# Kernel tuning notes

Measured on AMD Instinct MI355X. Metric: run time of the kernel, lower is better.

The kernel has to match this reference:

```python
import jax, jax.numpy as jnp
import numpy as np

N = 20000          # nodes
E_RAND = 320000    # random edges (avg degree 16)
E = E_RAND + N     # + self loops (no 0-in-degree nodes)
F_IN = 128
H1, D1 = 8, 32     # layer-1 heads / per-head dim
N_CLS = 40
NEG_SLOPE = 0.2


def setup_inputs() -> dict:
    key = jax.random.key(0)
    ks = jax.random.split(key, 9)
    x = jax.random.normal(ks[0], (N, F_IN), jnp.float32)
    src = jnp.concatenate([jax.random.randint(ks[1], (E_RAND,), 0, N),
                           jnp.arange(N)]).astype(jnp.int32)
    dst = jnp.concatenate([jax.random.randint(ks[2], (E_RAND,), 0, N),
                           jnp.arange(N)]).astype(jnp.int32)
    W1 = jax.random.normal(ks[3], (F_IN, H1 * D1), jnp.float32) / np.sqrt(F_IN)
    attn_l1 = jax.random.normal(ks[4], (H1, D1), jnp.float32) * 0.1
    attn_r1 = jax.random.normal(ks[5], (H1, D1), jnp.float32) * 0.1
    W2 = jax.random.normal(ks[6], (H1 * D1, N_CLS), jnp.float32) / np.sqrt(H1 * D1)
    attn_l2 = jax.random.normal(ks[7], (1, N_CLS), jnp.float32) * 0.1
    attn_r2 = jax.random.normal(ks[8], (1, N_CLS), jnp.float32) * 0.1
    return {"x": x, "W1": W1, "attn_l1": attn_l1, "attn_r1": attn_r1,
            "W2": W2, "attn_l2": attn_l2, "attn_r2": attn_r2,
            "src": src, "dst": dst}


def gat_layer(h, W, attn_l, attn_r, src, dst, n_nodes):
    """DGL GATConv (aggr='mean' path), eval mode (dropout = identity)."""
    H, D = attn_l.shape
    ft = (h @ W).reshape(-1, H, D)                 # [N, H, D]
    el = jnp.sum(ft * attn_l, axis=-1)             # [N, H]
    er = jnp.sum(ft * attn_r, axis=-1)             # [N, H]
    e = jax.nn.leaky_relu(el[src] + er[dst], NEG_SLOPE)   # [E, H]
    # ragged softmax over incoming edges of each dst node
    m = jax.ops.segment_max(e, dst, num_segments=n_nodes)
    m = jnp.where(jnp.isfinite(m), m, 0.0)         # guard empty segments
    ex = jnp.exp(e - m[dst])                       # [E, H]
    s = jax.ops.segment_sum(ex, dst, num_segments=n_nodes)
    alpha = ex / jnp.maximum(s[dst], 1e-16)        # [E, H]
    # weighted sum of src features
    out = jax.ops.segment_sum(ft[src] * alpha[:, :, None], dst,
                              num_segments=n_nodes)  # [N, H, D]
    return out


def reference(x, W1, attn_l1, attn_r1, W2, attn_l2, attn_r2, src, dst):
    h = gat_layer(x, W1, attn_l1, attn_r1, src, dst, N)   # [N, 8, 32]
    h = jax.nn.relu(h).reshape(N, H1 * D1)                # flatten(1)
    out = gat_layer(h, W2, attn_l2, attn_r2, src, dst, N) # [N, 1, 40]
    return out.mean(axis=1)                               # [N, 40]
```

## Files before the change

### kernel.cpp

```cpp
#include <hip/hip_runtime.h>
#include <hip/hip_fp16.h>

#define FIN 128
#define F1 256
#define H1N 8
#define D1N 32
#define NCLS 40
#define FT2P 64
#define W2PITCH 260
#define NEG 0.2f

static __device__ __forceinline__ float leaky(float x){ return x >= 0.f ? x : NEG*x; }

__global__ void k_hist(const int* __restrict__ dst, int* __restrict__ deg, int E){
    int e = blockIdx.x*256 + threadIdx.x;
    if (e < E) atomicAdd(&deg[dst[e]], 1);
}

__global__ void k_scan1(const int* __restrict__ deg, int* __restrict__ rowptr,
                        int* __restrict__ bsum, int n){
    __shared__ int s[256];
    int t = threadIdx.x;
    int i = blockIdx.x*256 + t;
    int v = (i < n) ? deg[i] : 0;
    s[t] = v;
    __syncthreads();
    for (int off=1; off<256; off<<=1){
        int y = (t >= off) ? s[t-off] : 0;
        __syncthreads();
        if (t >= off) s[t] += y;
        __syncthreads();
    }
    if (i < n) rowptr[i] = s[t] - v;
    if (t == 255) bsum[blockIdx.x] = s[255];
}

__global__ void k_scan2(int* __restrict__ rowptr, const int* __restrict__ bsum,
                        int n, int E){
    int b = blockIdx.x;
    int l = threadIdx.x & 63;
    int v = 0;
    for (int j = l; j < b; j += 64) v += bsum[j];
    for (int msk=1; msk<64; msk<<=1) v += __shfl_xor(v, msk);
    int i = b*256 + threadIdx.x;
    if (i < n) rowptr[i] += v;
    else if (i == n) rowptr[n] = E;
}

__global__ void k_scatter(const int* __restrict__ src, const int* __restrict__ dst,
                          const int* __restrict__ rowptr, int* __restrict__ deg,
                          int* __restrict__ adj, int E){
    int e = blockIdx.x*256 + threadIdx.x;
    if (e < E){
        int d = dst[e];
        int pos = atomicSub(&deg[d], 1) - 1;
        adj[rowptr[d] + pos] = src[e];
    }
}

__global__ __launch_bounds__(256) void k_gemm1(const float* __restrict__ X,
                                               const float* __restrict__ W,
                                               const float* __restrict__ al,
                                               const float* __restrict__ ar,
                                               __half* __restrict__ FT,
                                               float* __restrict__ el,
                                               float* __restrict__ er, int M){
    __shared__ float As[32][68];
    __shared__ float Bs[32][68];
    int t = threadIdx.x;
    int bx = blockIdx.x & 3;
    int by = blockIdx.x >> 2;
    int m0 = by*64, n0 = bx*64;
    int ty = t >> 4, tx = t & 15;
    float acc[4][4] = {};
    for (int k0 = 0; k0 < FIN; k0 += 32){
        #pragma unroll
        for (int p=0;p<2;p++){
            int f = t + p*256;
            int m = f >> 3;
            int kq = f & 7;
            int row = m0 + m;
            float4 v = make_float4(0.f,0.f,0.f,0.f);
            if (row < M) v = *(const float4*)&X[row*FIN + k0 + kq*4];
            As[kq*4+0][m] = v.x; As[kq*4+1][m] = v.y;
            As[kq*4+2][m] = v.z; As[kq*4+3][m] = v.w;
        }
        #pragma unroll
        for (int p=0;p<2;p++){
            int f = t + p*256;
            int kk = f >> 4;
            int nq = f & 15;
            float4 v = *(const float4*)&W[(size_t)(k0+kk)*F1 + n0 + nq*4];
            *(float4*)&Bs[kk][nq*4] = v;
        }
        __syncthreads();
        #pragma unroll
        for (int kk=0; kk<32; kk++){
            float4 a4 = *(const float4*)&As[kk][ty*4];
            float4 b4 = *(const float4*)&Bs[kk][tx*4];
            float av[4] = {a4.x,a4.y,a4.z,a4.w};
            float bv[4] = {b4.x,b4.y,b4.z,b4.w};
            #pragma unroll
            for (int r=0;r<4;r++)
                #pragma unroll
                for (int c=0;c<4;c++)
                    acc[r][c] = fmaf(av[r], bv[c], acc[r][c]);
        }
        __syncthreads();
    }
    int h = (bx<<1) + (tx>>3);
    int basew = h*D1N + (tx&7)*4;
    float4 wl = *(const float4*)&al[basew];
    float4 wr = *(const float4*)&ar[basew];
    float pl[4], pr[4];
    #pragma unroll
    for (int r=0;r<4;r++){
        pl[r] = acc[r][0]*wl.x + acc[r][1]*wl.y + acc[r][2]*wl.z + acc[r][3]*wl.w;
        pr[r] = acc[r][0]*wr.x + acc[r][1]*wr.y + acc[r][2]*wr.z + acc[r][3]*wr.w;
    }
    #pragma unroll
    for (int msk=1; msk<8; msk<<=1){
        #pragma unroll
        for (int r=0;r<4;r++){
            pl[r] += __shfl_xor(pl[r], msk);
            pr[r] += __shfl_xor(pr[r], msk);
        }
    }
    #pragma unroll
    for (int r=0;r<4;r++){
        int row = m0 + ty*4 + r;
        if (row < M){
            union { uint2 u; __half2 h2[2]; } P;
            P.h2[0] = __floats2half2_rn(acc[r][0], acc[r][1]);
            P.h2[1] = __floats2half2_rn(acc[r][2], acc[r][3]);
            *(uint2*)&FT[(size_t)row*F1 + n0 + tx*4] = P.u;
            if ((tx & 7) == 0){
                el[row*H1N + h] = pl[r];
                er[row*H1N + h] = pr[r];
            }
        }
    }
}

__global__ __launch_bounds__(256) void k_agg1(const __half* __restrict__ FT,
                      const float* __restrict__ el, const float* __restrict__ er,
                      const float* __restrict__ W2,
                      const float* __restrict__ al2, const float* __restrict__ ar2,
                      const int* __restrict__ rowptr, const int* __restrict__ adj,
                      __half* __restrict__ FT2, float* __restrict__ el2,
                      float* __restrict__ er2, int n, int nwTot){
    __shared__ __half W2h[40*W2PITCH];
    __shared__ float  hst[4][260];
    int t = threadIdx.x;
    for (int e = t; e < 256*40; e += 256){
        int k = e / 40, c = e - k*40;
        W2h[c*W2PITCH + k] = __float2half_rn(W2[e]);
    }
    __syncthreads();

    int w = t >> 6, l = t & 63;
    int h = l & 7, je = l >> 3;
    int h2 = l >> 3;
    int c = (l < 40) ? l : (l - 40);
    float keep = (l < NCLS) ? 1.f : 0.f;
    float a2l = al2[c], a2r = ar2[c];
    const __half* wrow = &W2h[c*W2PITCH];
    float* hp = &hst[w][0];

    for (int node = blockIdx.x*4 + w; node < n; node += nwTot){
        int rs = rowptr[node];
        int deg = rowptr[node+1] - rs;

        float erh = er[node*H1N + h];
        float m = -1e30f, ssum = 0.f;
        for (int j0 = 0; j0 < deg; j0 += 8){
            int j = j0 + je;
            if (j < deg){
                int s = adj[rs + j];
                float e = leaky(el[s*H1N + h] + erh);
                if (e > m){ ssum = ssum*__expf(m - e) + 1.f; m = e; }
                else ssum += __expf(e - m);
            }
        }
        #pragma unroll
        for (int msk=8; msk<64; msk<<=1){
            float m2 = __shfl_xor(m, msk);
            float s2 = __shfl_xor(ssum, msk);
            float nm = fmaxf(m, m2);
            ssum = ssum*__expf(m - nm) + s2*__expf(m2 - nm);
            m = nm;
        }

        float m2 = __shfl(m, h2);
        float s2 = __shfl(ssum, h2);
        float inv = 1.f / fmaxf(s2, 1e-16f);
        float erh2 = er[node*H1N + h2];
        float ax=0.f, ay=0.f, az=0.f, aw=0.f;
        int j = 0;
        for (; j + 8 <= deg; j += 8){
            int sv[8];
            #pragma unroll
            for (int i=0;i<8;i++) sv[i] = adj[rs+j+i];
            float av[8];
            #pragma unroll
            for (int i=0;i<8;i++)
                av[i] = __expf(leaky(el[sv[i]*H1N + h2] + erh2) - m2);
            #pragma unroll
            for (int i=0;i<8;i++){
                union { uint2 u; __half2 h2v[2]; } U;
                U.u = *(const uint2*)&FT[(size_t)sv[i]*F1 + l*4];
                float2 f01 = __half22float2(U.h2v[0]);
                float2 f23 = __half22float2(U.h2v[1]);
                ax = fmaf(av[i], f01.x, ax); ay = fmaf(av[i], f01.y, ay);
                az = fmaf(av[i], f23.x, az); aw = fmaf(av[i], f23.y, aw);
            }
        }
        for (; j < deg; j++){
            int s = adj[rs + j];
            float a = __expf(leaky(el[s*H1N + h2] + erh2) - m2);
            union { uint2 u; __half2 h2v[2]; } U;
            U.u = *(const uint2*)&FT[(size_t)s*F1 + l*4];
            float2 f01 = __half22float2(U.h2v[0]);
            float2 f23 = __half22float2(U.h2v[1]);
            ax = fmaf(a, f01.x, ax); ay = fmaf(a, f01.y, ay);
            az = fmaf(a, f23.x, az); aw = fmaf(a, f23.y, aw);
        }
        ax = fmaxf(ax*inv, 0.f); ay = fmaxf(ay*inv, 0.f);
        az = fmaxf(az*inv, 0.f); aw = fmaxf(aw*inv, 0.f);

        *(float4*)&hp[l*4] = make_float4(ax, ay, az, aw);
        __builtin_amdgcn_wave_barrier();
        asm volatile("s_waitcnt lgkmcnt(0)" ::: "memory");
        float out = 0.f;
        #pragma unroll 8
        for (int k0 = 0; k0 < 64; k0++){
            float4 hv = *(const float4*)&hp[k0*4];
            __half2 wa = *(const __half2*)&wrow[k0*4];
            __half2 wb = *(const __half2*)&wrow[k0*4+2];
            float2 fa = __half22float2(wa), fb = __half22float2(wb);
            out = fmaf(hv.x, fa.x, out); out = fmaf(hv.y, fa.y, out);
            out = fmaf(hv.z, fb.x, out); out = fmaf(hv.w, fb.y, out);
        }
        __builtin_amdgcn_wave_barrier();
        float pl = keep * out * a2l;
        float pr = keep * out * a2r;
        #pragma unroll
        for (int msk=1; msk<64; msk<<=1){
            pl += __shfl_xor(pl, msk);
            pr += __shfl_xor(pr, msk);
        }
        if (l == 0){ el2[node] = pl; er2[node] = pr; }
        if (l < NCLS) FT2[(size_t)node*FT2P + l] = __float2half_rn(out);
    }
}

__global__ __launch_bounds__(256) void k_agg2(const __half* __restrict__ FT2,
                      const float* __restrict__ el, const float* __restrict__ er,
                      const int* __restrict__ rowptr, const int* __restrict__ adj,
                      float* __restrict__ out, int n){
    int node = (blockIdx.x*256 + threadIdx.x) >> 6;
    int l = threadIdx.x & 63;
    if (node >= n) return;
    int rs = rowptr[node];
    int deg = rowptr[node+1] - rs;
    float ern = er[node];
    float m = -1e30f, ssum = 0.f;
    for (int j = l; j < deg; j += 64){
        int s = adj[rs + j];
        float e = leaky(el[s] + ern);
        if (e > m){ ssum = ssum*__expf(m - e) + 1.f; m = e; }
        else ssum += __expf(e - m);
    }
    #pragma unroll
    for (int msk=1; msk<64; msk<<=1){
        float mm = __shfl_xor(m, msk);
        float s2 = __shfl_xor(ssum, msk);
        float nm = fmaxf(m, mm);
        ssum = ssum*__expf(m - nm) + s2*__expf(mm - nm);
        m = nm;
    }
    float inv = 1.f / fmaxf(ssum, 1e-16f);
    float acc = 0.f;
    int j = 0;
    for (; j + 8 <= deg; j += 8){
        int sv[8];
        #pragma unroll
        for (int i=0;i<8;i++) sv[i] = adj[rs+j+i];
        float av[8];
        #pragma unroll
        for (int i=0;i<8;i++)
            av[i] = __expf(leaky(el[sv[i]] + ern) - m);
        if (l < NCLS){
            #pragma unroll
            for (int i=0;i<8;i++){
                float f = __half2float(FT2[(size_t)sv[i]*FT2P + l]);
                acc = fmaf(av[i], f, acc);
            }
        }
    }
    for (; j < deg; j++){
        int s = adj[rs + j];
        float a = __expf(leaky(el[s] + ern) - m);
        if (l < NCLS) acc = fmaf(a, __half2float(FT2[(size_t)s*FT2P + l]), acc);
    }
    if (l < NCLS) out[(size_t)node*NCLS + l] = acc * inv;
}

extern "C" void kernel_launch(void* const* d_in, const int* in_sizes, int n_in,
                              void* d_out, int out_size, void* d_ws, size_t ws_size,
                              hipStream_t stream){
    const float* x   = (const float*)d_in[0];
    const float* W1  = (const float*)d_in[1];
    const float* al1 = (const float*)d_in[2];
    const float* ar1 = (const float*)d_in[3];
    const float* W2  = (const float*)d_in[4];
    const float* al2 = (const float*)d_in[5];
    const float* ar2 = (const float*)d_in[6];
    const int*   src = (const int*)d_in[7];
    const int*   dst = (const int*)d_in[8];
    int E = in_sizes[7];
    int n = in_sizes[0] / FIN;

    char* ws = (char*)d_ws;
    size_t off = 0;
    auto alloc = [&](size_t bytes)->void*{
        void* p = ws + off; off += (bytes + 255) & ~(size_t)255; return p;
    };
    __half* ft1h  = (__half*)alloc((size_t)n*F1*2);
    __half* ft2h  = (__half*)alloc((size_t)n*FT2P*2);
    float*  el1   = (float*)alloc((size_t)n*H1N*4);
    float*  er1   = (float*)alloc((size_t)n*H1N*4);
    float*  el2   = (float*)alloc((size_t)n*4);
    float*  er2   = (float*)alloc((size_t)n*4);
    int*    rowptr= (int*)alloc((size_t)(n+1)*4);
    int*    adj   = (int*)alloc((size_t)E*4);
    int*    bsum  = (int*)alloc((size_t)((n+255)/256)*4);
    int*    deg   = (int*)alloc((size_t)n*4);

    int nb_e = (E + 255)/256;
    int nb_n = (n + 255)/256;

    hipMemsetAsync(deg, 0, (size_t)n*4, stream);
    k_hist   <<<nb_e, 256, 0, stream>>>(dst, deg, E);
    k_scan1  <<<nb_n, 256, 0, stream>>>(deg, rowptr, bsum, n);
    k_scan2  <<<(n+1+255)/256, 256, 0, stream>>>(rowptr, bsum, n, E);
    k_scatter<<<nb_e, 256, 0, stream>>>(src, dst, rowptr, deg, adj, E);

    k_gemm1  <<<((n+63)/64)*4, 256, 0, stream>>>(x, W1, al1, ar1, ft1h, el1, er1, n);

    int aggBlocks = 2500;
    k_agg1   <<<aggBlocks, 256, 0, stream>>>(ft1h, el1, er1, W2, al2, ar2,
                                             rowptr, adj, ft2h, el2, er2,
                                             n, aggBlocks*4);
    k_agg2   <<<(n+3)/4, 256, 0, stream>>>(ft2h, el2, er2, rowptr, adj,
                                           (float*)d_out, n);
}
```

Before: 212.1 us.

## Drop softmax max-subtraction pass, use 512-thread agg blocks and split dot accumulators

After: 215.0 us. About the same (+1.4%).

```diff
diff --git a/kernel.cpp b/kernel.cpp
--- a/kernel.cpp
+++ b/kernel.cpp
@@ -7,7 +7,7 @@
 #define D1N 32
 #define NCLS 40
 #define FT2P 64
-#define W2PITCH 260
+#define W2PITCH 258
 #define NEG 0.2f
 
 static __device__ __forceinline__ float leaky(float x){ return x >= 0.f ? x : NEG*x; }
@@ -142,7 +142,7 @@
     }
 }
 
-__global__ __launch_bounds__(256) void k_agg1(const __half* __restrict__ FT,
+__global__ __launch_bounds__(512) void k_agg1(const __half* __restrict__ FT,
                       const float* __restrict__ el, const float* __restrict__ er,
                       const float* __restrict__ W2,
                       const float* __restrict__ al2, const float* __restrict__ ar2,
@@ -150,16 +150,15 @@
                       __half* __restrict__ FT2, float* __restrict__ el2,
                       float* __restrict__ er2, int n, int nwTot){
     __shared__ __half W2h[40*W2PITCH];
-    __shared__ float  hst[4][260];
+    __shared__ float  hst[8][260];
     int t = threadIdx.x;
-    for (int e = t; e < 256*40; e += 256){
+    for (int e = t; e < 256*40; e += 512){
         int k = e / 40, c = e - k*40;
         W2h[c*W2PITCH + k] = __float2half_rn(W2[e]);
     }
     __syncthreads();
 
     int w = t >> 6, l = t & 63;
-    int h = l & 7, je = l >> 3;
     int h2 = l >> 3;
     int c = (l < 40) ? l : (l - 40);
     float keep = (l < NCLS) ? 1.f : 0.f;
@@ -167,34 +166,12 @@
     const __half* wrow = &W2h[c*W2PITCH];
     float* hp = &hst[w][0];
 
-    for (int node = blockIdx.x*4 + w; node < n; node += nwTot){
+    for (int node = blockIdx.x*8 + w; node < n; node += nwTot){
         int rs = rowptr[node];
         int deg = rowptr[node+1] - rs;
-
-        float erh = er[node*H1N + h];
-        float m = -1e30f, ssum = 0.f;
-        for (int j0 = 0; j0 < deg; j0 += 8){
-            int j = j0 + je;
-            if (j < deg){
-                int s = adj[rs + j];
-                float e = leaky(el[s*H1N + h] + erh);
-                if (e > m){ ssum = ssum*__expf(m - e) + 1.f; m = e; }
-                else ssum += __expf(e - m);
-            }
-        }
-        #pragma unroll
-        for (int msk=8; msk<64; msk<<=1){
-            float m2 = __shfl_xor(m, msk);
-            float s2 = __shfl_xor(ssum, msk);
-            float nm = fmaxf(m, m2);
-            ssum = ssum*__expf(m - nm) + s2*__expf(m2 - nm);
-            m = nm;
-        }
-
-        float m2 = __shfl(m, h2);
-        float s2 = __shfl(ssum, h2);
-        float inv = 1.f / fmaxf(s2, 1e-16f);
         float erh2 = er[node*H1N + h2];
+
+        float ssum = 0.f;
         float ax=0.f, ay=0.f, az=0.f, aw=0.f;
         int j = 0;
         for (; j + 8 <= deg; j += 8){
@@ -203,8 +180,10 @@
             for (int i=0;i<8;i++) sv[i] = adj[rs+j+i];
             float av[8];
             #pragma unroll
-            for (int i=0;i<8;i++)
-                av[i] = __expf(leaky(el[sv[i]*H1N + h2] + erh2) - m2);
+            for (int i=0;i<8;i++){
+                av[i] = __expf(leaky(el[sv[i]*H1N + h2] + erh2));
+                ssum += av[i];
+            }
             #pragma unroll
             for (int i=0;i<8;i++){
                 union { uint2 u; __half2 h2v[2]; } U;
@@ -217,7 +196,8 @@
         }
         for (; j < deg; j++){
             int s = adj[rs + j];
-            float a = __expf(leaky(el[s*H1N + h2] + erh2) - m2);
+            float a = __expf(leaky(el[s*H1N + h2] + erh2));
+            ssum += a;
             union { uint2 u; __half2 h2v[2]; } U;
             U.u = *(const uint2*)&FT[(size_t)s*F1 + l*4];
             float2 f01 = __half22float2(U.h2v[0]);
@@ -225,22 +205,38 @@
             ax = fmaf(a, f01.x, ax); ay = fmaf(a, f01.y, ay);
             az = fmaf(a, f23.x, az); aw = fmaf(a, f23.y, aw);
         }
+        float inv = 1.f / fmaxf(ssum, 1e-16f);
         ax = fmaxf(ax*inv, 0.f); ay = fmaxf(ay*inv, 0.f);
         az = fmaxf(az*inv, 0.f); aw = fmaxf(aw*inv, 0.f);
 
         *(float4*)&hp[l*4] = make_float4(ax, ay, az, aw);
         __builtin_amdgcn_wave_barrier();
         asm volatile("s_waitcnt lgkmcnt(0)" ::: "memory");
-        float out = 0.f;
-        #pragma unroll 8
-        for (int k0 = 0; k0 < 64; k0++){
-            float4 hv = *(const float4*)&hp[k0*4];
-            __half2 wa = *(const __half2*)&wrow[k0*4];
-            __half2 wb = *(const __half2*)&wrow[k0*4+2];
-            float2 fa = __half22float2(wa), fb = __half22float2(wb);
-            out = fmaf(hv.x, fa.x, out); out = fmaf(hv.y, fa.y, out);
-            out = fmaf(hv.z, fb.x, out); out = fmaf(hv.w, fb.y, out);
-        }
+        float o0=0.f, o1=0.f, o2=0.f, o3=0.f;
+        #pragma unroll
+        for (int k0 = 0; k0 < 64; k0 += 4){
+            {   float4 hv = *(const float4*)&hp[k0*4];
+                float2 fa = __half22float2(*(const __half2*)&wrow[k0*4]);
+                float2 fb = __half22float2(*(const __half2*)&wrow[k0*4+2]);
+                o0 = fmaf(hv.x, fa.x, o0); o0 = fmaf(hv.y, fa.y, o0);
+                o0 = fmaf(hv.z, fb.x, o0); o0 = fmaf(hv.w, fb.y, o0); }
+            {   float4 hv = *(const float4*)&hp[(k0+1)*4];
+                float2 fa = __half22float2(*(const __half2*)&wrow[(k0+1)*4]);
+                float2 fb = __half22float2(*(const __half2*)&wrow[(k0+1)*4+2]);
+                o1 = fmaf(hv.x, fa.x, o1); o1 = fmaf(hv.y, fa.y, o1);
+                o1 = fmaf(hv.z, fb.x, o1); o1 = fmaf(hv.w, fb.y, o1); }
+            {   float4 hv = *(const float4*)&hp[(k0+2)*4];
+                float2 fa = __half22float2(*(const __half2*)&wrow[(k0+2)*4]);
+                float2 fb = __half22float2(*(const __half2*)&wrow[(k0+2)*4+2]);
+                o2 = fmaf(hv.x, fa.x, o2); o2 = fmaf(hv.y, fa.y, o2);
+                o2 = fmaf(hv.z, fb.x, o2); o2 = fmaf(hv.w, fb.y, o2); }
+            {   float4 hv = *(const float4*)&hp[(k0+3)*4];
+                float2 fa = __half22float2(*(const __half2*)&wrow[(k0+3)*4]);
+                float2 fb = __half22float2(*(const __half2*)&wrow[(k0+3)*4+2]);
+                o3 = fmaf(hv.x, fa.x, o3); o3 = fmaf(hv.y, fa.y, o3);
+                o3 = fmaf(hv.z, fb.x, o3); o3 = fmaf(hv.w, fb.y, o3); }
+        }
+        float out = (o0 + o1) + (o2 + o3);
         __builtin_amdgcn_wave_barrier();
         float pl = keep * out * a2l;
         float pr = keep * out * a2r;
@@ -264,23 +260,7 @@
     int rs = rowptr[node];
     int deg = rowptr[node+1] - rs;
     float ern = er[node];
-    float m = -1e30f, ssum = 0.f;
-    for (int j = l; j < deg; j += 64){
-        int s = adj[rs + j];
-        float e = leaky(el[s] + ern);
-        if (e > m){ ssum = ssum*__expf(m - e) + 1.f; m = e; }
-        else ssum += __expf(e - m);
-    }
-    #pragma unroll
-    for (int msk=1; msk<64; msk<<=1){
-        float mm = __shfl_xor(m, msk);
-        float s2 = __shfl_xor(ssum, msk);
-        float nm = fmaxf(m, mm);
-        ssum = ssum*__expf(m - nm) + s2*__expf(mm - nm);
-        m = nm;
-    }
-    float inv = 1.f / fmaxf(ssum, 1e-16f);
-    float acc = 0.f;
+    float ssum = 0.f, acc = 0.f;
     int j = 0;
     for (; j + 8 <= deg; j += 8){
         int sv[8];
@@ -288,8 +268,10 @@
         for (int i=0;i<8;i++) sv[i] = adj[rs+j+i];
         float av[8];
         #pragma unroll
-        for (int i=0;i<8;i++)
-            av[i] = __expf(leaky(el[sv[i]] + ern) - m);
+        for (int i=0;i<8;i++){
+            av[i] = __expf(leaky(el[sv[i]] + ern));
+            ssum += av[i];
+        }
         if (l < NCLS){
             #pragma unroll
             for (int i=0;i<8;i++){
@@ -300,10 +282,11 @@
     }
     for (; j < deg; j++){
         int s = adj[rs + j];
-        float a = __expf(leaky(el[s] + ern) - m);
+        float a = __expf(leaky(el[s] + ern));
+        ssum += a;
         if (l < NCLS) acc = fmaf(a, __half2float(FT2[(size_t)s*FT2P + l]), acc);
     }
-    if (l < NCLS) out[(size_t)node*NCLS + l] = acc * inv;
+    if (l < NCLS) out[(size_t)node*NCLS + l] = acc / fmaxf(ssum, 1e-16f);
 }
 
 extern "C" void kernel_launch(void* const* d_in, const int* in_sizes, int n_in,
@@ -348,10 +331,10 @@
 
     k_gemm1  <<<((n+63)/64)*4, 256, 0, stream>>>(x, W1, al1, ar1, ft1h, el1, er1, n);
 
-    int aggBlocks = 2500;
-    k_agg1   <<<aggBlocks, 256, 0, stream>>>(ft1h, el1, er1, W2, al2, ar2,
+    int aggBlocks = 1250;
+    k_agg1   <<<aggBlocks, 512, 0, stream>>>(ft1h, el1, er1, W2, al2, ar2,
                                              rowptr, adj, ft2h, el2, er2,
-                                             n, aggBlocks*4);
+                                             n, aggBlocks*8);
     k_agg2   <<<(n+3)/4, 256, 0, stream>>>(ft2h, el2, er2, rowptr, adj,
                                            (float*)d_out, n);
 }
```
